# Optimization experiments

Hardware: AMD Instinct MI355X
Metric: run time of the kernel (lower is better)

## Reference

```python
import jax, jax.numpy as jnp
import numpy as np

DIM = 64        # block channel width
D3 = DIM * 3    # high-freq (HL,LH,HH) channels
HEADS = 6       # D3 // 32
WS = 8          # window size
SHIFT = 4       # shift size
HID = 128       # int(dim * ffn_expansion_factor)
PATCH = 8       # PSFFN spectral patch size


def _relative_position_index(ws):
    coords = np.stack(np.meshgrid(np.arange(ws), np.arange(ws), indexing='ij'))
    cf = coords.reshape(2, -1)
    rel = (cf[:, :, None] - cf[:, None, :]).transpose(1, 2, 0).astype(np.int64)
    rel[:, :, 0] += ws - 1
    rel[:, :, 1] += ws - 1
    rel[:, :, 0] *= 2 * ws - 1
    return rel.sum(-1).astype(np.int32)  # (ws*ws, ws*ws)


def _ln(x, w, b, eps=1e-6):
    # LayerNorm over channel dim of NCHW
    mu = x.mean(1, keepdims=True)
    var = x.var(1, keepdims=True)
    return (x - mu) * jax.lax.rsqrt(var + eps) * w[None, :, None, None] + b[None, :, None, None]


def _conv1x1(x, w):  # w: (O, I)
    return jnp.einsum('bihw,oi->bohw', x, w)


def _dwconv3(x, w):  # depthwise 3x3, w: (C,1,3,3)
    return jax.lax.conv_general_dilated(
        x, w, (1, 1), ((1, 1), (1, 1)),
        dimension_numbers=('NCHW', 'OIHW', 'NCHW'),
        feature_group_count=x.shape[1])


def _gelu(x):
    return jax.nn.gelu(x, approximate=False)


def _dwt(x):
    x01 = x[:, :, 0::2, :] / 2.0
    x02 = x[:, :, 1::2, :] / 2.0
    x1 = x01[:, :, :, 0::2]; x2 = x02[:, :, :, 0::2]
    x3 = x01[:, :, :, 1::2]; x4 = x02[:, :, :, 1::2]
    ll = x1 + x2 + x3 + x4
    high = jnp.concatenate([-x1 - x2 + x3 + x4, -x1 + x2 - x3 + x4, x1 - x2 - x3 + x4], axis=1)
    return ll, high


def _iwt(ll, high):
    C = ll.shape[1]
    hl, lh, hh = jnp.split(high, 3, axis=1)
    x1 = (ll - hl - lh + hh) / 2.0
    x2 = (ll - hl + lh - hh) / 2.0
    x3 = (ll + hl - lh - hh) / 2.0
    x4 = (ll + hl + lh + hh) / 2.0
    b, _, h, w = ll.shape
    even_rows = jnp.stack([x1, x3], axis=-1)  # (b,C,h,w,2) col parity
    odd_rows = jnp.stack([x2, x4], axis=-1)
    T = jnp.stack([even_rows, odd_rows], axis=3)  # (b,C,h,2,w,2)
    return T.reshape(b, C, 2 * h, 2 * w)


def _swmhsa(x, w_qkv, b_qkv, w_proj, b_proj, rel_table, rel_idx):
    B, C, H, W = x.shape
    d = C // HEADS
    xh = x.transpose(0, 2, 3, 1)                         # NHWC
    xh = jnp.roll(xh, (-SHIFT, -SHIFT), axis=(1, 2))
    nh, nw = H // WS, W // WS
    xw = xh.reshape(B, nh, WS, nw, WS, C).transpose(0, 1, 3, 2, 4, 5)
    xw = xw.reshape(B * nh * nw, WS * WS, C)             # (N, 64, C)
    qkv = xw @ w_qkv.T + b_qkv                           # (N, 64, 3C)
    qkv = qkv.reshape(-1, WS * WS, 3, HEADS, d).transpose(2, 0, 3, 1, 4)
    q, k, v = qkv[0], qkv[1], qkv[2]                     # (N, h, 64, d)
    bias = rel_table[rel_idx.reshape(-1)].reshape(WS * WS, WS * WS, HEADS).transpose(2, 0, 1)
    attn = jnp.einsum('nhqd,nhkd->nhqk', q, k) * (d ** -0.5) + bias[None]
    attn = jax.nn.softmax(attn, axis=-1)
    out = jnp.einsum('nhqk,nhkd->nhqd', attn, v).transpose(0, 2, 1, 3)
    out = out.reshape(B, nh, nw, WS, WS, C).transpose(0, 1, 3, 2, 4, 5).reshape(B, H, W, C)
    out = jnp.roll(out, (SHIFT, SHIFT), axis=(1, 2))
    out = out @ w_proj.T + b_proj
    return out.transpose(0, 3, 1, 2)


def _lhmsa(x, lnh_w, lnh_b, w_qkv, b_qkv, w_proj, b_proj, rel_table,
           gamma_main, gamma_aux, gamma_cross, aux_dw, aux_pw, cg_w1, cg_w2,
           attn_out_w, rel_idx):
    ll, high = _dwt(x)                                   # ll: (b,64,H/2,W/2); high: (b,192,...)
    high_norm = _ln(high, lnh_w, lnh_b)
    refined_high = high + gamma_main * _swmhsa(high_norm, w_qkv, b_qkv, w_proj, b_proj, rel_table, rel_idx)
    aux = _conv1x1(_gelu(_dwconv3(ll, aux_dw)), aux_pw)
    refined_ll = ll + gamma_aux * aux
    gap = ll.mean((2, 3))                                # (b,64)
    gate = jax.nn.sigmoid(_gelu(gap @ cg_w1.T) @ cg_w2.T)  # (b,192)
    refined_high = refined_high * (1.0 + gamma_cross * (gate[:, :, None, None] - 0.5) * 2.0)
    out = _iwt(refined_ll, refined_high)
    return _conv1x1(out - x, attn_out_w)


def _psffn(x, ffn_in_w, ffn_dw, ffn_out_w, w_base_real, w_base_imag):
    h = _dwconv3(_conv1x1(x, ffn_in_w), ffn_dw)
    x1, x2 = jnp.split(h, 2, axis=1)                     # (b,HID,H,W) each
    b, c, H, W = x1.shape
    p = PATCH
    xp = x1.reshape(b, c, H // p, p, W // p, p).transpose(0, 1, 2, 4, 3, 5)  # b c nh nw p p
    xf = jnp.fft.rfft2(xp)
    xf = xf * (w_base_real + 1j * w_base_imag)[None]     # (1,c,1,1,p,p//2+1) broadcast
    x1 = jnp.fft.irfft2(xf, s=(p, p)).astype(x.dtype)
    x1 = x1.transpose(0, 1, 2, 4, 3, 5).reshape(b, c, H, W)
    return _conv1x1(_gelu(x1) * x2, ffn_out_w)


def setup_inputs() -> dict:
    key = jax.random.key(0)
    ks = iter(jax.random.split(key, 32))
    s = 0.02
    inp = {}
    inp['x'] = jax.random.normal(next(ks), (4, DIM, 256, 256), dtype=jnp.float32)
    inp['ln_w'] = jnp.ones((DIM,), jnp.float32)
    inp['ln_b'] = jnp.zeros((DIM,), jnp.float32)
    inp['lnh_w'] = jnp.ones((D3,), jnp.float32)
    inp['lnh_b'] = jnp.zeros((D3,), jnp.float32)
    inp['w_qkv'] = s * jax.random.normal(next(ks), (3 * D3, D3), jnp.float32)
    inp['b_qkv'] = jnp.zeros((3 * D3,), jnp.float32)
    inp['w_proj'] = s * jax.random.normal(next(ks), (D3, D3), jnp.float32)
    inp['b_proj'] = jnp.zeros((D3,), jnp.float32)
    inp['rel_table'] = s * jax.random.normal(next(ks), ((2 * WS - 1) ** 2, HEADS), jnp.float32)
    inp['gamma_main'] = jnp.full((1,), 1e-4, jnp.float32)
    inp['gamma_aux'] = jnp.full((1,), 0.5, jnp.float32)
    inp['gamma_cross'] = jnp.full((1,), 1e-5, jnp.float32)
    inp['aux_dw'] = s * jax.random.normal(next(ks), (DIM, 1, 3, 3), jnp.float32)
    inp['aux_pw'] = s * jax.random.normal(next(ks), (DIM, DIM), jnp.float32)
    inp['cg_w1'] = s * jax.random.normal(next(ks), (DIM // 4 * 3, DIM), jnp.float32)  # dim*3//4=48
    inp['cg_w2'] = s * jax.random.normal(next(ks), (D3, DIM // 4 * 3), jnp.float32)
    inp['attn_out_w'] = s * jax.random.normal(next(ks), (DIM, DIM), jnp.float32)
    inp['ffn_in_w'] = s * jax.random.normal(next(ks), (2 * HID, DIM), jnp.float32)
    inp['ffn_dw'] = s * jax.random.normal(next(ks), (2 * HID, 1, 3, 3), jnp.float32)
    inp['ffn_out_w'] = s * jax.random.normal(next(ks), (DIM, HID), jnp.float32)
    inp['w_base_real'] = jnp.ones((HID, 1, 1, PATCH, PATCH // 2 + 1), jnp.float32)
    inp['w_base_imag'] = jnp.zeros((HID, 1, 1, PATCH, PATCH // 2 + 1), jnp.float32)
    inp['rel_idx'] = jnp.asarray(_relative_position_index(WS))
    return inp


def reference(x, ln_w, ln_b, lnh_w, lnh_b, w_qkv, b_qkv, w_proj, b_proj, rel_table,
              gamma_main, gamma_aux, gamma_cross, aux_dw, aux_pw, cg_w1, cg_w2,
              attn_out_w, ffn_in_w, ffn_dw, ffn_out_w, w_base_real, w_base_imag, rel_idx):
    x = x + _lhmsa(x, lnh_w, lnh_b, w_qkv, b_qkv, w_proj, b_proj, rel_table,
                   gamma_main, gamma_aux, gamma_cross, aux_dw, aux_pw, cg_w1, cg_w2,
                   attn_out_w, rel_idx)
    x = x + _psffn(_ln(x, ln_w, ln_b), ffn_in_w, ffn_dw, ffn_out_w, w_base_real, w_base_imag)
    return x
```

## Files before the change

### kernel.cpp

```cpp
#include <hip/hip_runtime.h>
#include <hip/hip_bf16.h>
#include <math.h>

#define DIMC 64
#define C3 192
#define NHEADS 6
#define DH 32
#define WSZ 8
#define SHIFTV 4
#define HIDC 128
#define FULLR 256
#define HALFR 128

typedef __attribute__((ext_vector_type(8))) short bf16x8;
typedef __attribute__((ext_vector_type(4))) float f32x4;

__device__ __forceinline__ float gelu_f(float x){
    return 0.5f * x * (1.0f + erff(x * 0.70710678118654752440f));
}
__device__ __forceinline__ unsigned short f2bf(float f){
    union { float f; unsigned u; } v; v.f = f;
    unsigned r = (v.u + 0x7FFF + ((v.u >> 16) & 1)) >> 16;
    return (unsigned short)r;
}
__device__ __forceinline__ float bf2f(unsigned short h){
    union { unsigned u; float f; } v; v.u = ((unsigned)h) << 16;
    return v.f;
}

__global__ __launch_bounds__(256) void k_dwt(const float* __restrict__ x, unsigned short* __restrict__ ll,
                                             unsigned short* __restrict__ high, float* __restrict__ gap,
                                             int nb, int b0){
    __shared__ float red[256];
    int idx = blockIdx.x * 256 + threadIdx.x;
    int total = nb << 19;
    if (idx >= total) return;
    int w4 = idx & 63;
    int h  = (idx >> 6) & 127;
    int c  = (idx >> 13) & 63;
    int b  = idx >> 19;
    const float* xp = x + (((size_t)(b0 + b) * DIMC + c) * FULLR + 2*h) * FULLR + 4*w4;
    float4 r0 = *(const float4*)xp;
    float4 r1 = *(const float4*)(xp + FULLR);
    size_t lbase = (((size_t)b*64 + c) << 14) + h*128 + w4*2;
    float x1a = 0.5f*r0.x, x3a = 0.5f*r0.y, x2a = 0.5f*r1.x, x4a = 0.5f*r1.y;
    float x1b = 0.5f*r0.z, x3b = 0.5f*r0.w, x2b = 0.5f*r1.z, x4b = 0.5f*r1.w;
    float lva = x1a + x2a + x3a + x4a;
    float lvb = x1b + x2b + x3b + x4b;
    *(unsigned*)&ll[lbase] = (unsigned)f2bf(lva) | ((unsigned)f2bf(lvb) << 16);
    int hs = (h + SHIFTV) & 127;  int wh = hs >> 3; int rr = hs & 7;
    int ws = (2*w4 + SHIFTV) & 127; int ww = ws >> 3; int cc = ws & 7;
    size_t wbase = ((size_t)(b*256 + wh*16 + ww)) * 12288 + rr*8 + cc;
    unsigned u;
    u = (unsigned)f2bf(-x1a - x2a + x3a + x4a) | ((unsigned)f2bf(-x1b - x2b + x3b + x4b) << 16);
    *(unsigned*)&high[wbase + (size_t)c*64] = u;
    u = (unsigned)f2bf(-x1a + x2a - x3a + x4a) | ((unsigned)f2bf(-x1b + x2b - x3b + x4b) << 16);
    *(unsigned*)&high[wbase + (size_t)(64 + c)*64] = u;
    u = (unsigned)f2bf( x1a - x2a - x3a + x4a) | ((unsigned)f2bf( x1b - x2b - x3b + x4b) << 16);
    *(unsigned*)&high[wbase + (size_t)(128 + c)*64] = u;
    red[threadIdx.x] = lva + lvb;
    __syncthreads();
    for (int st = 128; st > 0; st >>= 1){
        if (threadIdx.x < st) red[threadIdx.x] += red[threadIdx.x + st];
        __syncthreads();
    }
    if (threadIdx.x == 0) atomicAdd(&gap[b*64 + c], red[0]);
}

__global__ __launch_bounds__(256) void k_gate(const float* __restrict__ gap, const float* __restrict__ w1,
                                              const float* __restrict__ w2, float* __restrict__ gate){
    int b = blockIdx.x;
    __shared__ float hid[48];
    __shared__ float g[64];
    if (threadIdx.x < 64) g[threadIdx.x] = gap[b*64 + threadIdx.x] * (1.0f/16384.0f);
    __syncthreads();
    if (threadIdx.x < 48){
        float s = 0.f;
        for (int c = 0; c < 64; c++) s += g[c] * w1[threadIdx.x*64 + c];
        hid[threadIdx.x] = gelu_f(s);
    }
    __syncthreads();
    if (threadIdx.x < C3){
        float s = 0.f;
        for (int j = 0; j < 48; j++) s += hid[j] * w2[threadIdx.x*48 + j];
        gate[b*C3 + threadIdx.x] = 1.0f / (1.0f + expf(-s));
    }
}

__global__ __launch_bounds__(256) void k_cvt(const float* __restrict__ wq, const float* __restrict__ wp,
    const float* __restrict__ rel_table, const int* __restrict__ rel_idx, const float* __restrict__ wo,
    const float* __restrict__ wi, const float* __restrict__ wao, const float* __restrict__ pwa,
    unsigned short* __restrict__ wqb, unsigned short* __restrict__ wpb, float* __restrict__ bias6,
    unsigned short* __restrict__ wob, unsigned short* __restrict__ wib,
    unsigned short* __restrict__ waob, unsigned short* __restrict__ pwab, float* __restrict__ gap){
    int idx = blockIdx.x*256 + threadIdx.x;
    if (idx < 576*192) wqb[idx] = f2bf(wq[idx]);
    if (idx < 192*192) wpb[idx] = f2bf(wp[idx]);
    if (idx < 64*128)  wob[idx] = f2bf(wo[idx]);
    if (idx < 256*64)  wib[idx] = f2bf(wi[idx]);
    if (idx < 64*64){  waob[idx] = f2bf(wao[idx]); pwab[idx] = f2bf(pwa[idx]); }
    if (idx < 256)     gap[idx] = 0.f;
    if (idx < 6*64*64){
        int h = idx >> 12; int ij = idx & 4095;
        bias6[idx] = rel_table[rel_idx[ij]*NHEADS + h];
    }
}

__global__ __launch_bounds__(256) void k_kcirc(const float* __restrict__ wr, const float* __restrict__ wi,
                                               unsigned short* __restrict__ circ){
    __shared__ float ksl[64];
    int ch = blockIdx.x;
    int tid = threadIdx.x;
    if (tid < 64){
        int r = tid >> 3, c = tid & 7;
        float s = 0.f;
        for (int u = 0; u < 8; u++){
            for (int v = 0; v < 8; v++){
                float re, im;
                if (v <= 4){ re = wr[ch*40 + u*5 + v]; im = wi[ch*40 + u*5 + v]; }
                else { int u2 = (8-u)&7; int v2 = 8-v; re = wr[ch*40 + u2*5 + v2]; im = -wi[ch*40 + u2*5 + v2]; }
                float ang = (float)(u*r + v*c) * 0.78539816339744831f;
                float cs, sn; __sincosf(ang, &sn, &cs);
                s += re * cs - im * sn;
            }
        }
        ksl[tid] = s * (1.0f/64.0f);
    }
    __syncthreads();
    for (int idx = tid; idx < 4096; idx += 256){
        int o = idx >> 6, i = idx & 63;
        int dr = ((o >> 3) - (i >> 3)) & 7;
        int dc = ((o & 7) - (i & 7)) & 7;
        circ[(size_t)ch*4096 + idx] = f2bf(ksl[dr*8 + dc]);
    }
}

__global__ __launch_bounds__(256, 3) void k_attn(unsigned short* __restrict__ high,
    const unsigned short* __restrict__ wqb, const unsigned short* __restrict__ wpb,
    const float* __restrict__ bqkv, const float* __restrict__ bproj,
    const float* __restrict__ bias6, const float* __restrict__ lnw, const float* __restrict__ lnb,
    const float* __restrict__ gate, const float* __restrict__ gm_p, const float* __restrict__ gc_p)
{
    __shared__ __align__(16) unsigned short xb[64][200];
    __shared__ __align__(16) unsigned short qs[64][40];
    __shared__ __align__(16) unsigned short ks2[64][40];
    __shared__ __align__(16) unsigned short vt[32][72];
    __shared__ __align__(16) unsigned short ps[64][72];
    __shared__ float st_s[4][64], st_ss[4][64];
    __shared__ float mu_s[64], rs_s[64];

    int tid = threadIdx.x;
    int lane = tid & 63;
    int wv = tid >> 6;
    int lrow = lane & 15;
    int lkg  = lane >> 4;
    int blk = blockIdx.x;
    int b  = blk >> 8;
    size_t wbase = (size_t)blk * 12288;
    const float scale = 0.17677669529663687f;
    float gm = gm_p[0], gc = gc_p[0];

    int t = lane, part = wv;
    float vals[48];
    {
        float s = 0.f, ss = 0.f;
        #pragma unroll
        for (int i = 0; i < 48; i++){
            float v = bf2f(high[wbase + (size_t)(part*48 + i)*64 + t]);
            vals[i] = v; s += v; ss += v*v;
        }
        st_s[part][t] = s; st_ss[part][t] = ss;
    }
    __syncthreads();
    if (tid < 64){
        float s = st_s[0][tid]+st_s[1][tid]+st_s[2][tid]+st_s[3][tid];
        float ss = st_ss[0][tid]+st_ss[1][tid]+st_ss[2][tid]+st_ss[3][tid];
        float mu = s*(1.f/C3);
        float var = ss*(1.f/C3) - mu*mu;
        mu_s[tid] = mu; rs_s[tid] = rsqrtf(var + 1e-6f);
    }
    __syncthreads();
    {
        float mu = mu_s[t], rs = rs_s[t];
        #pragma unroll
        for (int i8 = 0; i8 < 6; i8++){
            bf16x8 pk;
            #pragma unroll
            for (int jj = 0; jj < 8; jj++){
                int c = part*48 + i8*8 + jj;
                float nv = (vals[i8*8+jj] - mu) * rs * lnw[c] + lnb[c];
                pk[jj] = (short)f2bf(nv);
            }
            *(bf16x8*)&xb[t][part*48 + i8*8] = pk;
        }
    }
    __syncthreads();

    f32x4 pacc[3][4];
    #pragma unroll
    for (int mt3 = 0; mt3 < 3; mt3++)
        #pragma unroll
        for (int nt = 0; nt < 4; nt++) pacc[mt3][nt] = (f32x4){0.f,0.f,0.f,0.f};

    for (int h = 0; h < NHEADS; h++){
        f32x4 acc[6];
        #pragma unroll
        for (int nt = 0; nt < 6; nt++) acc[nt] = (f32x4){0.f,0.f,0.f,0.f};
        __builtin_amdgcn_s_setprio(1);
        for (int ksU = 0; ksU < 6; ksU++){
            int c0 = ksU*32 + lkg*8;
            bf16x8 a = *(const bf16x8*)&xb[wv*16 + lrow][c0];
            #pragma unroll
            for (int nt = 0; nt < 6; nt++){
                int which = nt >> 1;
                int gr = which*C3 + h*32 + (nt&1)*16 + lrow;
                bf16x8 bb = *(const bf16x8*)&wqb[(size_t)gr*C3 + c0];
                acc[nt] = __builtin_amdgcn_mfma_f32_16x16x32_bf16(a, bb, acc[nt], 0, 0, 0);
            }
        }
        __builtin_amdgcn_s_setprio(0);
        #pragma unroll
        for (int nt = 0; nt < 6; nt++){
            int which = nt >> 1;
            int d = (nt&1)*16 + lrow;
            float bias = bqkv[which*C3 + h*32 + d];
            #pragma unroll
            for (int r = 0; r < 4; r++){
                int row = wv*16 + lkg*4 + r;
                float v = acc[nt][r] + bias;
                if (which == 0)      qs[row][d]  = f2bf(v * scale);
                else if (which == 1) ks2[row][d] = f2bf(v);
                else                 vt[d][row]  = f2bf(v);
            }
        }
        __syncthreads();

        f32x4 sacc[4];
        {
            bf16x8 a = *(const bf16x8*)&qs[wv*16 + lrow][lkg*8];
            #pragma unroll
            for (int nt = 0; nt < 4; nt++){
                bf16x8 bb = *(const bf16x8*)&ks2[nt*16 + lrow][lkg*8];
                f32x4 z = (f32x4){0.f,0.f,0.f,0.f};
                sacc[nt] = __builtin_amdgcn_mfma_f32_16x16x32_bf16(a, bb, z, 0, 0, 0);
            }
        }
        {
            #pragma unroll
            for (int r = 0; r < 4; r++){
                int i = wv*16 + lkg*4 + r;
                float pv[4];
                float s = 0.f;
                #pragma unroll
                for (int nt = 0; nt < 4; nt++){
                    pv[nt] = __expf(sacc[nt][r] + bias6[h*4096 + i*64 + nt*16 + lrow]);
                    s += pv[nt];
                }
                s += __shfl_xor(s, 1); s += __shfl_xor(s, 2);
                s += __shfl_xor(s, 4); s += __shfl_xor(s, 8);
                float inv = 1.0f / s;
                #pragma unroll
                for (int nt = 0; nt < 4; nt++) ps[i][nt*16 + lrow] = f2bf(pv[nt] * inv);
            }
        }
        __syncthreads();

        f32x4 oacc[2];
        #pragma unroll
        for (int nt = 0; nt < 2; nt++) oacc[nt] = (f32x4){0.f,0.f,0.f,0.f};
        #pragma unroll
        for (int kst = 0; kst < 2; kst++){
            bf16x8 a = *(const bf16x8*)&ps[wv*16 + lrow][kst*32 + lkg*8];
            #pragma unroll
            for (int nt = 0; nt < 2; nt++){
                bf16x8 bb = *(const bf16x8*)&vt[nt*16 + lrow][kst*32 + lkg*8];
                oacc[nt] = __builtin_amdgcn_mfma_f32_16x16x32_bf16(a, bb, oacc[nt], 0, 0, 0);
            }
        }
        #pragma unroll
        for (int nt = 0; nt < 2; nt++)
            #pragma unroll
            for (int r = 0; r < 4; r++)
                qs[wv*16 + lkg*4 + r][nt*16 + lrow] = f2bf(oacc[nt][r]);
        __syncthreads();

        __builtin_amdgcn_s_setprio(1);
        #pragma unroll
        for (int mt3 = 0; mt3 < 3; mt3++){
            int o = wv*48 + mt3*16 + lrow;
            bf16x8 a = *(const bf16x8*)&wpb[(size_t)o*C3 + h*32 + lkg*8];
            #pragma unroll
            for (int nt = 0; nt < 4; nt++){
                bf16x8 bb = *(const bf16x8*)&qs[nt*16 + lrow][lkg*8];
                pacc[mt3][nt] = __builtin_amdgcn_mfma_f32_16x16x32_bf16(a, bb, pacc[mt3][nt], 0, 0, 0);
            }
        }
        __builtin_amdgcn_s_setprio(0);
        __syncthreads();
    }

    #pragma unroll
    for (int mt3 = 0; mt3 < 3; mt3++){
        #pragma unroll
        for (int r = 0; r < 4; r++){
            int o = wv*48 + mt3*16 + lkg*4 + r;
            float bias = bproj[o];
            float gf = 1.0f + gc * (gate[b*C3 + o] - 0.5f) * 2.0f;
            #pragma unroll
            for (int nt = 0; nt < 4; nt++){
                int token = nt*16 + lrow;
                size_t gi = wbase + (size_t)o*64 + token;
                float orig = bf2f(high[gi]);
                high[gi] = f2bf((orig + gm*(pacc[mt3][nt][r] + bias)) * gf);
            }
        }
    }
}

__global__ __launch_bounds__(256) void k_aux(const unsigned short* __restrict__ ll,
    const float* __restrict__ dw, const unsigned short* __restrict__ pwab, const float* __restrict__ ga_p,
    unsigned short* __restrict__ rll, int nb)
{
    __shared__ __align__(16) unsigned short sll[64][3][80];
    __shared__ __align__(16) unsigned short tlb[64][72];
    int tid = threadIdx.x;
    int blk = blockIdx.x;
    int b   = blk >> 8;
    int row = (blk >> 1) & 127;
    int seg = blk & 1;
    int px0 = seg*64;

    for (int j = tid; j < 1920; j += 256){
        int c = j / 30;
        int rem = j % 30;
        int dy = rem / 10;
        int i8 = rem % 10;
        int gr = row + dy - 1;
        int gp = px0 - 8 + i8*8;
        bf16x8 v = (bf16x8){0,0,0,0,0,0,0,0};
        if (gr >= 0 && gr < 128 && gp >= 0 && gp < 128)
            v = *(const bf16x8*)&ll[(((size_t)b*64 + c) << 14) + gr*128 + gp];
        *(bf16x8*)&sll[c][dy][i8*8] = v;
    }
    __syncthreads();

    int px = tid & 63, cq = tid >> 6;
    for (int ci = cq; ci < 64; ci += 4){
        const float* wd = dw + ci*9;
        float s = 0.f;
        #pragma unroll
        for (int dy = 0; dy < 3; dy++){
            float a0 = bf2f(sll[ci][dy][px+7]);
            float a1 = bf2f(sll[ci][dy][px+8]);
            float a2 = bf2f(sll[ci][dy][px+9]);
            s += wd[dy*3+0]*a0 + wd[dy*3+1]*a1 + wd[dy*3+2]*a2;
        }
        tlb[px][ci] = f2bf(gelu_f(s));
    }
    __syncthreads();

    int lane = tid & 63;
    int wv = tid >> 6;
    int lrow = lane & 15;
    int lkg  = lane >> 4;
    float ga = ga_p[0];
    f32x4 acc[4];
    #pragma unroll
    for (int nt = 0; nt < 4; nt++) acc[nt] = (f32x4){0.f,0.f,0.f,0.f};
    #pragma unroll
    for (int kst = 0; kst < 2; kst++){
        bf16x8 a = *(const bf16x8*)&pwab[(size_t)(wv*16 + lrow)*64 + kst*32 + lkg*8];
        #pragma unroll
        for (int nt = 0; nt < 4; nt++){
            bf16x8 bb = *(const bf16x8*)&tlb[nt*16 + lrow][kst*32 + lkg*8];
            acc[nt] = __builtin_amdgcn_mfma_f32_16x16x32_bf16(a, bb, acc[nt], 0, 0, 0);
        }
    }
    #pragma unroll
    for (int nt = 0; nt < 4; nt++){
        #pragma unroll
        for (int r = 0; r < 4; r++){
            int o = wv*16 + lkg*4 + r;
            int pxx = nt*16 + lrow;
            float base = bf2f(sll[o][1][pxx + 8]);
            rll[(((size_t)b*64 + o) << 14) + row*128 + px0 + pxx] = f2bf(base + ga * acc[nt][r]);
        }
    }
}

__global__ __launch_bounds__(256) void k_iwt_proj(const unsigned short* __restrict__ rll,
    const unsigned short* __restrict__ high,
    const float* __restrict__ x, const unsigned short* __restrict__ waob,
    unsigned short* __restrict__ y1b, int nb, int b0){
    __shared__ __align__(16) unsigned short dbufT[64][72];
    __shared__ float xt[64][65];
    int tid = threadIdx.x;
    int blk = blockIdx.x;
    int seg = blk & 3;
    int ph  = (blk >> 2) & 255;
    int b   = blk >> 10;
    int pw0 = seg * 64;
    int h2 = ph >> 1, p = ph & 1;
    size_t xbase = ((size_t)(b0 + b) * DIMC) * 65536;
    int px = tid & 63;
    int ci = tid >> 6;
    int pwv = pw0 + px;
    int w2 = pwv >> 1, q = pwv & 1;
    float shl = q ? 1.f : -1.f;
    float slh = p ? 1.f : -1.f;
    float shh = (p == q) ? 1.f : -1.f;
    int hs = (h2 + SHIFTV) & 127; int wh = hs >> 3; int rr = hs & 7;
    int ws = (w2 + SHIFTV) & 127; int ww = ws >> 3; int cc = ws & 7;
    size_t wbase = ((size_t)(b*256 + wh*16 + ww)) * 12288 + rr*8 + cc;
    for (int i = ci; i < 64; i += 4){
        float llv = bf2f(rll[(((size_t)b*64 + i) << 14) + h2*128 + w2]);
        float hl = bf2f(high[wbase + (size_t)i*64]);
        float lh = bf2f(high[wbase + (size_t)(64 + i)*64]);
        float hh = bf2f(high[wbase + (size_t)(128 + i)*64]);
        float iw = 0.5f * (llv + shl*hl + slh*lh + shh*hh);
        float xv = x[xbase + (size_t)i*65536 + (size_t)ph*256 + pwv];
        xt[i][px] = xv;
        dbufT[px][i] = f2bf(iw - xv);
    }
    __syncthreads();
    int lane = tid & 63;
    int wv = tid >> 6;
    int lrow = lane & 15;
    int lkg  = lane >> 4;
    f32x4 acc[4];
    #pragma unroll
    for (int nt = 0; nt < 4; nt++) acc[nt] = (f32x4){0.f,0.f,0.f,0.f};
    #pragma unroll
    for (int kst = 0; kst < 2; kst++){
        bf16x8 a = *(const bf16x8*)&waob[(size_t)(wv*16 + lrow)*64 + kst*32 + lkg*8];
        #pragma unroll
        for (int nt = 0; nt < 4; nt++){
            bf16x8 bb = *(const bf16x8*)&dbufT[nt*16 + lrow][kst*32 + lkg*8];
            acc[nt] = __builtin_amdgcn_mfma_f32_16x16x32_bf16(a, bb, acc[nt], 0, 0, 0);
        }
    }
    #pragma unroll
    for (int nt = 0; nt < 4; nt++){
        #pragma unroll
        for (int r = 0; r < 4; r++){
            int o = wv*16 + lkg*4 + r;
            int pxx = nt*16 + lrow;
            y1b[(((size_t)(b*64 + o)) << 16) + (size_t)ph*256 + pw0 + pxx] =
                f2bf(xt[o][pxx] + acc[nt][r]);
        }
    }
}

__global__ __launch_bounds__(256) void k_ffn_a(const unsigned short* __restrict__ y1b,
    const float* __restrict__ lnw, const float* __restrict__ lnb,
    const unsigned short* __restrict__ wib, unsigned short* __restrict__ h, int nb)
{
    __shared__ float yl[64][72];
    __shared__ __align__(16) unsigned short xn[64][72];
    __shared__ __align__(16) unsigned short ho[128][72];
    __shared__ float mu_s[64], rs_s[64];
    int tid = threadIdx.x;
    int lane = tid & 63;
    int wv = tid >> 6;
    int lrow = lane & 15;
    int lkg  = lane >> 4;
    int blk = blockIdx.x;
    int b   = blk >> 10;
    int row = (blk >> 2) & 255;
    int q   = blk & 3;

    for (int idx = tid; idx < 512; idx += 256){
        int c = idx >> 3, p8 = idx & 7;
        bf16x8 v = *(const bf16x8*)&y1b[((size_t)(b*64 + c) << 16) + (size_t)row*256 + q*64 + p8*8];
        #pragma unroll
        for (int j = 0; j < 8; j++) yl[c][p8*8 + j] = bf2f((unsigned short)v[j]);
    }
    __syncthreads();
    if (tid < 64){
        float s = 0.f, ss = 0.f;
        for (int c = 0; c < 64; c++){ float v = yl[c][tid]; s += v; ss += v*v; }
        float mu = s * (1.f/64.f), var = ss * (1.f/64.f) - mu*mu;
        mu_s[tid] = mu; rs_s[tid] = rsqrtf(var + 1e-6f);
    }
    __syncthreads();
    for (int idx = tid; idx < 4096; idx += 256){
        int px = idx & 63, c = idx >> 6;
        xn[px][c] = f2bf((yl[c][px] - mu_s[px]) * rs_s[px] * lnw[c] + lnb[c]);
    }
    __syncthreads();

    for (int hh = 0; hh < 2; hh++){
        int oc0 = hh*128;
        f32x4 acc[8];
        #pragma unroll
        for (int nt = 0; nt < 8; nt++) acc[nt] = (f32x4){0.f,0.f,0.f,0.f};
        #pragma unroll
        for (int kst = 0; kst < 2; kst++){
            bf16x8 a = *(const bf16x8*)&xn[wv*16 + lrow][kst*32 + lkg*8];
            #pragma unroll
            for (int nt = 0; nt < 8; nt++){
                bf16x8 bb = *(const bf16x8*)&wib[(size_t)(oc0 + nt*16 + lrow)*64 + kst*32 + lkg*8];
                acc[nt] = __builtin_amdgcn_mfma_f32_16x16x32_bf16(a, bb, acc[nt], 0, 0, 0);
            }
        }
        #pragma unroll
        for (int nt = 0; nt < 8; nt++)
            #pragma unroll
            for (int r = 0; r < 4; r++)
                ho[nt*16 + lrow][wv*16 + lkg*4 + r] = f2bf(acc[nt][r]);
        __syncthreads();
        for (int idx = tid; idx < 1024; idx += 256){
            int oc = idx >> 3, p8 = idx & 7;
            bf16x8 v = *(const bf16x8*)&ho[oc][p8*8];
            *(bf16x8*)&h[(size_t)(b*256 + oc0 + oc)*65536 + (size_t)row*256 + q*64 + p8*8] = v;
        }
        __syncthreads();
    }
}

#define PMS 68
__global__ __launch_bounds__(256) void k_convb(const unsigned short* __restrict__ h,
    const float* __restrict__ w_dw, const unsigned short* __restrict__ circ,
    unsigned short* __restrict__ mbuf, int nb)
{
    __shared__ __align__(16) unsigned short stage[4][10][272];
    __shared__ __align__(16) unsigned short pm[4][32*PMS];
    int tid = threadIdx.x;
    int lane = tid & 63;
    int wv = tid >> 6;
    int lrow = lane & 15;
    int lkg  = lane >> 4;
    int blk = blockIdx.x;
    int b   = blk >> 9;
    int chg = (blk >> 5) & 15;
    int pc  = blk & 31;
    int r0 = pc*8;

    auto stage_fn = [&](int c16){
        int chA = chg*8 + c16;
        int chs[4] = {chA, chA+128, chA+4, chA+132};
        for (int j = tid; j < 1280; j += 256){
            int pl = j / 320;
            int rem = j - pl*320;
            int row10 = rem >> 5;
            int c0 = (rem & 31) << 3;
            int gr = r0 + row10 - 1;
            bf16x8 v = (bf16x8){0,0,0,0,0,0,0,0};
            if (gr >= 0 && gr < 256)
                v = *(const bf16x8*)&h[((size_t)(b*256 + chs[pl]) << 16) + (size_t)gr*256 + c0];
            *(bf16x8*)&stage[pl][row10][c0] = v;
        }
    };

    stage_fn(0);
    __syncthreads();

    for (int c16 = 0; c16 < 4; c16++){
        {
            int chA = chg*8 + c16;
            int chs[4] = {chA, chA+128, chA+4, chA+132};
            for (int j = tid; j < 1024; j += 256){
                int pl = j >> 8;
                int rem = j & 255;
                int r = rem >> 5;
                int c0 = (rem & 31) << 3;
                const float* wd = w_dw + chs[pl]*9;
                float acc[8] = {0,0,0,0,0,0,0,0};
                #pragma unroll
                for (int dy = 0; dy < 3; dy++){
                    const unsigned short* rp = &stage[pl][r+dy][0];
                    bf16x8 v = *(const bf16x8*)&rp[c0];
                    float vf[8];
                    #pragma unroll
                    for (int jj = 0; jj < 8; jj++) vf[jj] = bf2f((unsigned short)v[jj]);
                    float l  = (c0 > 0)   ? bf2f(rp[c0 - 1]) : 0.f;
                    float rg = (c0 < 248) ? bf2f(rp[c0 + 8]) : 0.f;
                    float w0 = wd[dy*3+0], w1 = wd[dy*3+1], w2 = wd[dy*3+2];
                    acc[0] += w0*l + w1*vf[0] + w2*vf[1];
                    #pragma unroll
                    for (int jj = 1; jj < 7; jj++) acc[jj] += w0*vf[jj-1] + w1*vf[jj] + w2*vf[jj+1];
                    acc[7] += w0*vf[6] + w1*vf[7] + w2*rg;
                }
                bf16x8 o;
                #pragma unroll
                for (int jj = 0; jj < 8; jj++) o[jj] = (short)f2bf(acc[jj]);
                *(bf16x8*)&pm[pl][(c0 >> 3)*PMS + r*8] = o;
            }
        }
        __syncthreads();
        if (c16 < 3) stage_fn(c16 + 1);
        {
            int spl = (wv & 1) * 2;
            int ch = chg*8 + (wv & 1)*4 + c16;
            const unsigned short* Bb = circ + (size_t)ch*4096;
            int plocal = (wv >> 1)*16;
            f32x4 acc4[4];
            #pragma unroll
            for (int nt = 0; nt < 4; nt++) acc4[nt] = (f32x4){0.f,0.f,0.f,0.f};
            #pragma unroll
            for (int kst = 0; kst < 2; kst++){
                bf16x8 a = *(const bf16x8*)&pm[spl][(plocal + lrow)*PMS + kst*32 + lkg*8];
                #pragma unroll
                for (int nt = 0; nt < 4; nt++){
                    bf16x8 bb = *(const bf16x8*)&Bb[(size_t)(nt*16 + lrow)*64 + kst*32 + lkg*8];
                    acc4[nt] = __builtin_amdgcn_mfma_f32_16x16x32_bf16(a, bb, acc4[nt], 0, 0, 0);
                }
            }
            unsigned short* Mb = mbuf + ((size_t)(b*128 + ch) << 16);
            #pragma unroll
            for (int nt = 0; nt < 4; nt++){
                #pragma unroll
                for (int r = 0; r < 4; r++){
                    int pl2 = plocal + lkg*4 + r;
                    int px = nt*16 + lrow;
                    float g = bf2f(pm[spl + 1][pl2*PMS + px]);
                    Mb[(size_t)(pc*32 + pl2)*64 + px] = f2bf(gelu_f(acc4[nt][r]) * g);
                }
            }
        }
        __syncthreads();
    }
}

__global__ __launch_bounds__(256) void k_out(const unsigned short* __restrict__ y1b,
    const unsigned short* __restrict__ mbuf, const unsigned short* __restrict__ wob,
    float* __restrict__ out, int b0)
{
    __shared__ __align__(16) unsigned short mlds[2][64][136];
    int tid = threadIdx.x;
    int lane = tid & 63;
    int wv = tid >> 6;
    int lrow = lane & 15;
    int lkg  = lane >> 4;
    int blk = blockIdx.x;
    int b  = blk >> 9;
    int pp = blk & 511;

    for (int it = 0; it < 8; it++){
        int chunk = tid + it*256;
        int ch = chunk >> 4;
        int p = (chunk >> 3) & 1;
        int px8 = chunk & 7;
        bf16x8 v = *(const bf16x8*)&mbuf[(((size_t)(b*128 + ch)) << 16) + (size_t)(2*pp + p)*64 + px8*8];
        #pragma unroll
        for (int j = 0; j < 8; j++) mlds[p][px8*8 + j][ch] = (unsigned short)v[j];
    }
    __syncthreads();

    int p = wv >> 1;
    int ochalf = wv & 1;
    f32x4 acc[2][4];
    #pragma unroll
    for (int mt = 0; mt < 2; mt++)
        #pragma unroll
        for (int nt = 0; nt < 4; nt++) acc[mt][nt] = (f32x4){0.f,0.f,0.f,0.f};
    #pragma unroll
    for (int kst = 0; kst < 4; kst++){
        bf16x8 a0 = *(const bf16x8*)&wob[(size_t)(ochalf*32 + 0  + lrow)*128 + kst*32 + lkg*8];
        bf16x8 a1 = *(const bf16x8*)&wob[(size_t)(ochalf*32 + 16 + lrow)*128 + kst*32 + lkg*8];
        #pragma unroll
        for (int nt = 0; nt < 4; nt++){
            bf16x8 bb = *(const bf16x8*)&mlds[p][nt*16 + lrow][kst*32 + lkg*8];
            acc[0][nt] = __builtin_amdgcn_mfma_f32_16x16x32_bf16(a0, bb, acc[0][nt], 0, 0, 0);
            acc[1][nt] = __builtin_amdgcn_mfma_f32_16x16x32_bf16(a1, bb, acc[1][nt], 0, 0, 0);
        }
    }
    int patchIdx = 2*pp + p;
    int Rb = (patchIdx >> 5) * 8, Cb = (patchIdx & 31) * 8;
    #pragma unroll
    for (int mt = 0; mt < 2; mt++){
        #pragma unroll
        for (int nt = 0; nt < 4; nt++){
            #pragma unroll
            for (int r = 0; r < 4; r++){
                int oc = ochalf*32 + mt*16 + lkg*4 + r;
                int px = nt*16 + lrow;
                int R = Rb + (px >> 3), C = Cb + (px & 7);
                size_t li = (((size_t)(b*64 + oc)) << 16) + (size_t)R*256 + C;
                size_t go = (((size_t)((b0 + b)*64 + oc)) << 16) + (size_t)R*256 + C;
                out[go] = bf2f(y1b[li]) + acc[mt][nt][r];
            }
        }
    }
}

extern "C" void kernel_launch(void* const* d_in, const int* in_sizes, int n_in,
                              void* d_out, int out_size, void* d_ws, size_t ws_size,
                              hipStream_t stream){
    const float* x        = (const float*)d_in[0];
    const float* ln_w     = (const float*)d_in[1];
    const float* ln_b     = (const float*)d_in[2];
    const float* lnh_w    = (const float*)d_in[3];
    const float* lnh_b    = (const float*)d_in[4];
    const float* w_qkv    = (const float*)d_in[5];
    const float* b_qkv    = (const float*)d_in[6];
    const float* w_proj   = (const float*)d_in[7];
    const float* b_proj   = (const float*)d_in[8];
    const float* rel_tab  = (const float*)d_in[9];
    const float* g_main   = (const float*)d_in[10];
    const float* g_aux    = (const float*)d_in[11];
    const float* g_cross  = (const float*)d_in[12];
    const float* aux_dw   = (const float*)d_in[13];
    const float* aux_pw   = (const float*)d_in[14];
    const float* cg_w1    = (const float*)d_in[15];
    const float* cg_w2    = (const float*)d_in[16];
    const float* attn_ow  = (const float*)d_in[17];
    const float* ffn_in_w = (const float*)d_in[18];
    const float* ffn_dw   = (const float*)d_in[19];
    const float* ffn_ow   = (const float*)d_in[20];
    const float* wb_re    = (const float*)d_in[21];
    const float* wb_im    = (const float*)d_in[22];
    const int*   rel_idx  = (const int*)d_in[23];
    float* out = (float*)d_out;
    (void)in_sizes; (void)n_in; (void)out_size;

    const size_t MBsz = (size_t)1 << 20;
    auto need = [&](int nb)->size_t { return (size_t)nb*72*MBsz + 2*MBsz; };
    int nbmax = 4;
    while (nbmax > 1 && need(nbmax) > ws_size) nbmax >>= 1;

    for (int b0 = 0; b0 < 4; b0 += nbmax){
        int nb = nbmax;
        char* p = (char*)d_ws;
        char* U = p;                      p += (size_t)nb*72*MBsz;
        float* gap  = (float*)p;          p += 4096;
        float* gate = (float*)p;          p += 4096;
        unsigned short* wqb = (unsigned short*)p; p += 576*192*2;
        unsigned short* wpb = (unsigned short*)p; p += 192*192*2;
        float* bias6 = (float*)p;         p += 6*64*64*4;
        unsigned short* circ = (unsigned short*)p; p += 128*4096*2;
        unsigned short* wob  = (unsigned short*)p; p += 64*128*2;
        unsigned short* wib  = (unsigned short*)p; p += 256*64*2;
        unsigned short* waob = (unsigned short*)p; p += 64*64*2;
        unsigned short* pwab = (unsigned short*)p; p += 64*64*2;

        unsigned short* ll   = (unsigned short*)U;
        unsigned short* highb= (unsigned short*)(U + (size_t)nb*2*MBsz);
        unsigned short* rll  = (unsigned short*)(U + (size_t)nb*8*MBsz);
        unsigned short* mbuf = (unsigned short*)U;
        unsigned short* h    = (unsigned short*)(U + (size_t)nb*32*MBsz);
        unsigned short* y1b  = (unsigned short*)(U + (size_t)nb*64*MBsz);

        k_kcirc<<<128, 256, 0, stream>>>(wb_re, wb_im, circ);
        k_cvt<<<432, 256, 0, stream>>>(w_qkv, w_proj, rel_tab, rel_idx, ffn_ow, ffn_in_w,
                                       attn_ow, aux_pw,
                                       wqb, wpb, bias6, wob, wib, waob, pwab, gap);
        k_dwt<<<nb*2048, 256, 0, stream>>>(x, ll, highb, gap, nb, b0);
        k_gate<<<nb, 256, 0, stream>>>(gap, cg_w1, cg_w2, gate);
        k_attn<<<nb*256, 256, 0, stream>>>(highb, wqb, wpb, b_qkv, b_proj, bias6,
                                           lnh_w, lnh_b, gate, g_main, g_cross);
        k_aux<<<nb*256, 256, 0, stream>>>(ll, aux_dw, pwab, g_aux, rll, nb);
        k_iwt_proj<<<nb*1024, 256, 0, stream>>>(rll, highb, x, waob, y1b, nb, b0);
        k_ffn_a<<<nb*1024, 256, 0, stream>>>(y1b, ln_w, ln_b, wib, h, nb);
        k_convb<<<nb*512, 256, 0, stream>>>(h, ffn_dw, circ, mbuf, nb);
        k_out<<<nb*512, 256, 0, stream>>>(y1b, mbuf, wob, out, b0);
    }
}
```

Measured before the change: 517.9 us.

## Fuse IWT projection with FFN LayerNorm and input projection; add MFMA priority hints

Merges k_iwt_proj and k_ffn_a into one kernel. The projected y1 tile is kept in registers and LDS, the LayerNorm statistics are computed with wave shuffles plus a cross-wave LDS reduction, and the FFN input 1x1 conv runs right away. This removes the re-read of y1b from global memory and one kernel launch, in exchange for more LDS per block and a longer kernel. It also wraps the MFMA loops in several kernels with s_setprio so those waves are favoured while issuing matrix instructions.

```diff
diff --git a/kernel.cpp b/kernel.cpp
--- a/kernel.cpp
+++ b/kernel.cpp
@@ -367,6 +367,7 @@
     f32x4 acc[4];
     #pragma unroll
     for (int nt = 0; nt < 4; nt++) acc[nt] = (f32x4){0.f,0.f,0.f,0.f};
+    __builtin_amdgcn_s_setprio(1);
     #pragma unroll
     for (int kst = 0; kst < 2; kst++){
         bf16x8 a = *(const bf16x8*)&pwab[(size_t)(wv*16 + lrow)*64 + kst*32 + lkg*8];
@@ -376,6 +377,7 @@
             acc[nt] = __builtin_amdgcn_mfma_f32_16x16x32_bf16(a, bb, acc[nt], 0, 0, 0);
         }
     }
+    __builtin_amdgcn_s_setprio(0);
     #pragma unroll
     for (int nt = 0; nt < 4; nt++){
         #pragma unroll
@@ -388,12 +390,21 @@
     }
 }
 
-__global__ __launch_bounds__(256) void k_iwt_proj(const unsigned short* __restrict__ rll,
-    const unsigned short* __restrict__ high,
-    const float* __restrict__ x, const unsigned short* __restrict__ waob,
-    unsigned short* __restrict__ y1b, int nb, int b0){
-    __shared__ __align__(16) unsigned short dbufT[64][72];
-    __shared__ float xt[64][65];
+__global__ __launch_bounds__(256) void k_iwt_ffn(const unsigned short* __restrict__ rll,
+    const unsigned short* __restrict__ high, const float* __restrict__ x,
+    const unsigned short* __restrict__ waob,
+    const float* __restrict__ lnw, const float* __restrict__ lnb,
+    const unsigned short* __restrict__ wib,
+    unsigned short* __restrict__ y1b, unsigned short* __restrict__ h, int nb, int b0)
+{
+    __shared__ __align__(16) char smem[38912];
+    float* xt            = (float*)smem;
+    unsigned short* ho   = (unsigned short*)smem;
+    unsigned short* dbufT= (unsigned short*)(smem + 18432);
+    unsigned short* xn   = (unsigned short*)(smem + 27648);
+    float* pss           = (float*)(smem + 36864);
+    float* psss          = (float*)(smem + 37888);
+
     int tid = threadIdx.x;
     int blk = blockIdx.x;
     int seg = blk & 3;
@@ -419,10 +430,11 @@
         float hh = bf2f(high[wbase + (size_t)(128 + i)*64]);
         float iw = 0.5f * (llv + shl*hl + slh*lh + shh*hh);
         float xv = x[xbase + (size_t)i*65536 + (size_t)ph*256 + pwv];
-        xt[i][px] = xv;
-        dbufT[px][i] = f2bf(iw - xv);
-    }
-    __syncthreads();
+        xt[i*65 + px] = xv;
+        dbufT[px*72 + i] = f2bf(iw - xv);
+    }
+    __syncthreads();
+
     int lane = tid & 63;
     int wv = tid >> 6;
     int lrow = lane & 15;
@@ -430,89 +442,87 @@
     f32x4 acc[4];
     #pragma unroll
     for (int nt = 0; nt < 4; nt++) acc[nt] = (f32x4){0.f,0.f,0.f,0.f};
+    __builtin_amdgcn_s_setprio(1);
     #pragma unroll
     for (int kst = 0; kst < 2; kst++){
         bf16x8 a = *(const bf16x8*)&waob[(size_t)(wv*16 + lrow)*64 + kst*32 + lkg*8];
         #pragma unroll
         for (int nt = 0; nt < 4; nt++){
-            bf16x8 bb = *(const bf16x8*)&dbufT[nt*16 + lrow][kst*32 + lkg*8];
+            bf16x8 bb = *(const bf16x8*)&dbufT[(nt*16 + lrow)*72 + kst*32 + lkg*8];
             acc[nt] = __builtin_amdgcn_mfma_f32_16x16x32_bf16(a, bb, acc[nt], 0, 0, 0);
         }
     }
+    __builtin_amdgcn_s_setprio(0);
+    float yv[4][4];
+    float s4[4], ss4[4];
+    #pragma unroll
+    for (int nt = 0; nt < 4; nt++){ s4[nt] = 0.f; ss4[nt] = 0.f; }
     #pragma unroll
     for (int nt = 0; nt < 4; nt++){
+        int pxx = nt*16 + lrow;
         #pragma unroll
         for (int r = 0; r < 4; r++){
             int o = wv*16 + lkg*4 + r;
-            int pxx = nt*16 + lrow;
-            y1b[(((size_t)(b*64 + o)) << 16) + (size_t)ph*256 + pw0 + pxx] =
-                f2bf(xt[o][pxx] + acc[nt][r]);
-        }
-    }
-}
-
-__global__ __launch_bounds__(256) void k_ffn_a(const unsigned short* __restrict__ y1b,
-    const float* __restrict__ lnw, const float* __restrict__ lnb,
-    const unsigned short* __restrict__ wib, unsigned short* __restrict__ h, int nb)
-{
-    __shared__ float yl[64][72];
-    __shared__ __align__(16) unsigned short xn[64][72];
-    __shared__ __align__(16) unsigned short ho[128][72];
-    __shared__ float mu_s[64], rs_s[64];
-    int tid = threadIdx.x;
-    int lane = tid & 63;
-    int wv = tid >> 6;
-    int lrow = lane & 15;
-    int lkg  = lane >> 4;
-    int blk = blockIdx.x;
-    int b   = blk >> 10;
-    int row = (blk >> 2) & 255;
-    int q   = blk & 3;
-
-    for (int idx = tid; idx < 512; idx += 256){
-        int c = idx >> 3, p8 = idx & 7;
-        bf16x8 v = *(const bf16x8*)&y1b[((size_t)(b*64 + c) << 16) + (size_t)row*256 + q*64 + p8*8];
-        #pragma unroll
-        for (int j = 0; j < 8; j++) yl[c][p8*8 + j] = bf2f((unsigned short)v[j]);
-    }
-    __syncthreads();
-    if (tid < 64){
-        float s = 0.f, ss = 0.f;
-        for (int c = 0; c < 64; c++){ float v = yl[c][tid]; s += v; ss += v*v; }
-        float mu = s * (1.f/64.f), var = ss * (1.f/64.f) - mu*mu;
-        mu_s[tid] = mu; rs_s[tid] = rsqrtf(var + 1e-6f);
-    }
-    __syncthreads();
-    for (int idx = tid; idx < 4096; idx += 256){
-        int px = idx & 63, c = idx >> 6;
-        xn[px][c] = f2bf((yl[c][px] - mu_s[px]) * rs_s[px] * lnw[c] + lnb[c]);
-    }
-    __syncthreads();
-
+            float v = xt[o*65 + pxx] + acc[nt][r];
+            yv[nt][r] = v;
+            s4[nt] += v; ss4[nt] += v*v;
+            y1b[(((size_t)(b*64 + o)) << 16) + (size_t)ph*256 + pw0 + pxx] = f2bf(v);
+        }
+    }
+    #pragma unroll
+    for (int nt = 0; nt < 4; nt++){
+        s4[nt]  += __shfl_xor(s4[nt], 16);  s4[nt]  += __shfl_xor(s4[nt], 32);
+        ss4[nt] += __shfl_xor(ss4[nt], 16); ss4[nt] += __shfl_xor(ss4[nt], 32);
+    }
+    if (lkg == 0){
+        #pragma unroll
+        for (int nt = 0; nt < 4; nt++){
+            pss[wv*64 + nt*16 + lrow]  = s4[nt];
+            psss[wv*64 + nt*16 + lrow] = ss4[nt];
+        }
+    }
+    __syncthreads();
+    #pragma unroll
+    for (int nt = 0; nt < 4; nt++){
+        int pxx = nt*16 + lrow;
+        float s  = pss[pxx]  + pss[64 + pxx]  + pss[128 + pxx]  + pss[192 + pxx];
+        float ss = psss[pxx] + psss[64 + pxx] + psss[128 + pxx] + psss[192 + pxx];
+        float mu = s * (1.f/64.f);
+        float var = ss * (1.f/64.f) - mu*mu;
+        float rs = rsqrtf(var + 1e-6f);
+        #pragma unroll
+        for (int r = 0; r < 4; r++){
+            int o = wv*16 + lkg*4 + r;
+            xn[pxx*72 + o] = f2bf((yv[nt][r] - mu) * rs * lnw[o] + lnb[o]);
+        }
+    }
+    __syncthreads();
     for (int hh = 0; hh < 2; hh++){
         int oc0 = hh*128;
-        f32x4 acc[8];
-        #pragma unroll
-        for (int nt = 0; nt < 8; nt++) acc[nt] = (f32x4){0.f,0.f,0.f,0.f};
+        f32x4 cacc[8];
+        #pragma unroll
+        for (int nt = 0; nt < 8; nt++) cacc[nt] = (f32x4){0.f,0.f,0.f,0.f};
+        __builtin_amdgcn_s_setprio(1);
         #pragma unroll
         for (int kst = 0; kst < 2; kst++){
-            bf16x8 a = *(const bf16x8*)&xn[wv*16 + lrow][kst*32 + lkg*8];
+            bf16x8 a = *(const bf16x8*)&xn[(wv*16 + lrow)*72 + kst*32 + lkg*8];
             #pragma unroll
             for (int nt = 0; nt < 8; nt++){
                 bf16x8 bb = *(const bf16x8*)&wib[(size_t)(oc0 + nt*16 + lrow)*64 + kst*32 + lkg*8];
-                acc[nt] = __builtin_amdgcn_mfma_f32_16x16x32_bf16(a, bb, acc[nt], 0, 0, 0);
-            }
-        }
+                cacc[nt] = __builtin_amdgcn_mfma_f32_16x16x32_bf16(a, bb, cacc[nt], 0, 0, 0);
+            }
+        }
+        __builtin_amdgcn_s_setprio(0);
         #pragma unroll
         for (int nt = 0; nt < 8; nt++)
             #pragma unroll
             for (int r = 0; r < 4; r++)
-                ho[nt*16 + lrow][wv*16 + lkg*4 + r] = f2bf(acc[nt][r]);
+                ho[(nt*16 + lrow)*72 + wv*16 + lkg*4 + r] = f2bf(cacc[nt][r]);
         __syncthreads();
         for (int idx = tid; idx < 1024; idx += 256){
             int oc = idx >> 3, p8 = idx & 7;
-            bf16x8 v = *(const bf16x8*)&ho[oc][p8*8];
-            *(bf16x8*)&h[(size_t)(b*256 + oc0 + oc)*65536 + (size_t)row*256 + q*64 + p8*8] = v;
+            bf16x8 v = *(const bf16x8*)&ho[oc*72 + p8*8];
+            *(bf16x8*)&h[(size_t)(b*256 + oc0 + oc)*65536 + (size_t)ph*256 + pw0 + p8*8] = v;
         }
         __syncthreads();
     }
@@ -597,6 +607,7 @@
             f32x4 acc4[4];
             #pragma unroll
             for (int nt = 0; nt < 4; nt++) acc4[nt] = (f32x4){0.f,0.f,0.f,0.f};
+            __builtin_amdgcn_s_setprio(1);
             #pragma unroll
             for (int kst = 0; kst < 2; kst++){
                 bf16x8 a = *(const bf16x8*)&pm[spl][(plocal + lrow)*PMS + kst*32 + lkg*8];
@@ -606,6 +617,7 @@
                     acc4[nt] = __builtin_amdgcn_mfma_f32_16x16x32_bf16(a, bb, acc4[nt], 0, 0, 0);
                 }
             }
+            __builtin_amdgcn_s_setprio(0);
             unsigned short* Mb = mbuf + ((size_t)(b*128 + ch) << 16);
             #pragma unroll
             for (int nt = 0; nt < 4; nt++){
@@ -654,6 +666,7 @@
     for (int mt = 0; mt < 2; mt++)
         #pragma unroll
         for (int nt = 0; nt < 4; nt++) acc[mt][nt] = (f32x4){0.f,0.f,0.f,0.f};
+    __builtin_amdgcn_s_setprio(1);
     #pragma unroll
     for (int kst = 0; kst < 4; kst++){
         bf16x8 a0 = *(const bf16x8*)&wob[(size_t)(ochalf*32 + 0  + lrow)*128 + kst*32 + lkg*8];
@@ -665,6 +678,7 @@
             acc[1][nt] = __builtin_amdgcn_mfma_f32_16x16x32_bf16(a1, bb, acc[1][nt], 0, 0, 0);
         }
     }
+    __builtin_amdgcn_s_setprio(0);
     int patchIdx = 2*pp + p;
     int Rb = (patchIdx >> 5) * 8, Cb = (patchIdx & 31) * 8;
     #pragma unroll
@@ -750,8 +764,8 @@
         k_attn<<<nb*256, 256, 0, stream>>>(highb, wqb, wpb, b_qkv, b_proj, bias6,
                                            lnh_w, lnh_b, gate, g_main, g_cross);
         k_aux<<<nb*256, 256, 0, stream>>>(ll, aux_dw, pwab, g_aux, rll, nb);
-        k_iwt_proj<<<nb*1024, 256, 0, stream>>>(rll, highb, x, waob, y1b, nb, b0);
-        k_ffn_a<<<nb*1024, 256, 0, stream>>>(y1b, ln_w, ln_b, wib, h, nb);
+        k_iwt_ffn<<<nb*1024, 256, 0, stream>>>(rll, highb, x, waob, ln_w, ln_b, wib,
+                                               y1b, h, nb, b0);
         k_convb<<<nb*512, 256, 0, stream>>>(h, ffn_dw, circ, mbuf, nb);
         k_out<<<nb*512, 256, 0, stream>>>(y1b, mbuf, wob, out, b0);
     }
```

Measured after the change: 495.8 us. -4.3%, faster.
